# Performance work log

Hardware: AMD Instinct MI355X
Metric: run time of the kernel (lower is better)

The kernel has to match this reference:

```python
import math
import jax, jax.numpy as jnp
import numpy as np

B, DIN, DOUT = 16384, 512, 512
LATERAL_K = 3
K_WTA = max(1, int(DOUT * 0.25))


def _build_L_mask(dout: int, k: int) -> np.ndarray:
    m = np.zeros((dout, dout), dtype=np.float32)
    for j in range(dout):
        nb = []
        for off in range(1, k + 1):
            if j - off >= 0:
                nb.append(j - off)
            if j + off < dout:
                nb.append(j + off)
        for n in nb[:k]:
            m[j, n] = 1.0
    return m


def _kwta_mask(x):
    # top-k winner-take-all mask along last dim (ties resolved like torch.topk)
    _, idx = jax.lax.top_k(x, K_WTA)
    rows = jnp.arange(x.shape[0])[:, None]
    return jnp.zeros_like(x).at[rows, idx].set(1.0)


def _phi(x, mask):
    return jax.nn.gelu(x, approximate=False) * mask


def _phi_deriv(x, mask):
    cdf = 0.5 * (1.0 + jax.lax.erf(x / math.sqrt(2.0)))
    pdf = jnp.exp(-0.5 * x * x) / math.sqrt(2.0 * math.pi)
    return (cdf + x * pdf) * mask


def _clip_update(d, max_norm):
    n = jnp.linalg.norm(d)  # global norm over the whole tensor, as in torch
    return jnp.where(n > max_norm, d * (max_norm / (n + 1e-8)), d)


def setup_inputs() -> dict:
    key = jax.random.key(0)
    ks = jax.random.split(key, 8)
    k_v = math.sqrt(1.0 / DIN)
    k_w = math.sqrt(1.0 / DOUT)
    return {
        "bottom_up": jax.random.normal(ks[0], (B, DIN), jnp.float32),
        "td_target": jax.random.normal(ks[1], (B, DOUT), jnp.float32) * 0.5,
        "x": jax.random.normal(ks[2], (B, DOUT), jnp.float32) * 0.5,
        "V": jax.random.uniform(ks[3], (DIN, DOUT), jnp.float32, -k_v, k_v),
        "b_in": jnp.full((DOUT,), -5.0, jnp.float32),
        "W_snap": jax.random.uniform(ks[4], (DOUT, DIN), jnp.float32, -k_w, k_w),
        "b_out_snap": jnp.zeros((DIN,), jnp.float32),
        "L": jax.random.uniform(ks[5], (DOUT, DOUT), jnp.float32, -0.1, 0.1),
        "L_mask": jnp.asarray(_build_L_mask(DOUT, LATERAL_K)),
        "step_i": 2,
    }


def reference(bottom_up, td_target, x, V, b_in, W_snap, b_out_snap, L, L_mask, step_i):
    tau, eta_x, lambda_act = 0.5, 0.8, 1e-6
    mask = _kwta_mask(x)
    phi_x = _phi(x, mask)                                     # [B, DOUT]
    prediction = phi_x @ W_snap + b_out_snap                  # [B, DIN]
    error = jax.lax.stop_gradient(bottom_up - prediction)     # detached in torch
    feedback_drive = (error @ W_snap.T) * _phi_deriv(x, mask)
    forward_drive = bottom_up @ V + b_in                      # [B, DOUT]
    recognition_drive = forward_drive - x                     # recognition_weight=1.0
    top_down_drive = 3.0 * (td_target - x)
    lateral_drive = phi_x @ (L * L_mask)
    state_grad = (feedback_drive + recognition_drive + top_down_drive
                  + 0.3 * lateral_drive - lambda_act * jnp.sign(x))
    eta = eta_x / (1.0 + 0.1 * step_i)
    dx = _clip_update(tau * eta * state_grad, 1.0)
    return jnp.clip(x + dx, -5.0, 5.0)
```

## Files before the change

### kernel.cpp

```cpp
#include <hip/hip_runtime.h>
#include <hip/hip_bf16.h>
#include <cstdint>


#define DEV static __device__ __forceinline__

typedef __attribute__((ext_vector_type(8))) short short8;
typedef __attribute__((ext_vector_type(4))) float f32x4;

static constexpr int BATCH = 16384;
static constexpr int D = 512;

DEV unsigned short f2bf(float f) {
  unsigned u = __float_as_uint(f);
  return (unsigned short)((u + 0x7FFFu + ((u >> 16) & 1u)) >> 16);
}
DEV float bf2f(unsigned short h) { return __uint_as_float(((unsigned)h) << 16); }

DEV float wsumf(float v) { for (int o = 32; o; o >>= 1) v += __shfl_xor(v, o, 64); return v; }

DEV void gload16(const void* g, void* l) {
  __builtin_amdgcn_global_load_lds((const __attribute__((address_space(1))) void*)g,
                                   (__attribute__((address_space(3))) void*)l, 16, 0, 0);
}

DEV void load8(const float* rowp, int lane, float v[8]) {
  const float4* q = (const float4*)rowp;
  float4 a = q[lane * 2], b = q[lane * 2 + 1];
  v[0] = a.x; v[1] = a.y; v[2] = a.z; v[3] = a.w;
  v[4] = b.x; v[5] = b.y; v[6] = b.z; v[7] = b.w;
}

__global__ __launch_bounds__(256) void prep_k(
    const float* __restrict__ W, const float* __restrict__ V,
    const float* __restrict__ L, const float* __restrict__ Lm,
    unsigned short* __restrict__ Wbt, unsigned short* __restrict__ Wb2,
    unsigned short* __restrict__ Vbt, float* __restrict__ Mc7,
    float* __restrict__ ssq)
{
  int idx = blockIdx.x * 256 + threadIdx.x;
  int n = idx >> 9, k = idx & 511;
  Wbt[idx] = f2bf(W[k * D + n]);
  Wb2[idx] = f2bf(W[idx]);
  Vbt[idx] = f2bf(V[k * D + n]);
  if (idx < 7 * D) {
    int t = idx >> 9, nn = idx & 511;
    int j = nn - 3 + t;
    float v = 0.f;
    if (j >= 0 && j < D && j != nn) v = L[j * D + nn] * Lm[j * D + nn];
    Mc7[idx] = v;
  }
  if (idx == 0) *ssq = 0.f;
}

__global__ __launch_bounds__(256) void kwta_k(
    const float* __restrict__ x, const float* __restrict__ td,
    const float* __restrict__ bu, const float* __restrict__ b_in,
    const float* __restrict__ Mc7,
    unsigned short* __restrict__ phi16, unsigned short* __restrict__ pd16,
    unsigned short* __restrict__ base16, unsigned short* __restrict__ bu16)
{
  __shared__ float pbuf[4][D];
  const int tid = threadIdx.x, lane = tid & 63, wv = tid >> 6;
  const int row = blockIdx.x * 4 + wv;
  const size_t rbase = (size_t)row * D;

  float xv[8];
  load8(x + rbase, lane, xv);
  unsigned key[8];
  #pragma unroll
  for (int s = 0; s < 8; ++s) {
    unsigned u = __float_as_uint(xv[s]);
    key[s] = (u & 0x80000000u) ? ~u : (u | 0x80000000u);
  }
  unsigned T = 0u;
  bool exact = false;
  for (int bit = 31; bit >= 0; --bit) {
    unsigned cand = T | (1u << bit);
    int c = 0;
    #pragma unroll
    for (int s = 0; s < 8; ++s) c += (int)__popcll(__ballot(key[s] >= cand));
    if (c == 128) { T = cand; exact = true; break; }
    if (c > 128) T = cand;
  }

  bool selv[8];
  if (exact) {
    #pragma unroll
    for (int s = 0; s < 8; ++s) selv[s] = (key[s] >= T);
  } else {
    int cg = 0;
    unsigned long long em[8];
    #pragma unroll
    for (int s = 0; s < 8; ++s) {
      cg += (int)__popcll(__ballot(key[s] > T));
      em[s] = __ballot(key[s] == T);
    }
    const int rneed = 128 - cg;
    const unsigned long long lower = (1ull << lane) - 1ull;
    int run = 0;
    #pragma unroll
    for (int s = 0; s < 8; ++s) run += (int)__popcll(em[s] & lower);
    #pragma unroll
    for (int s = 0; s < 8; ++s) {
      bool sel = key[s] > T;
      if (key[s] == T) { sel = (run < rneed); ++run; }
      selv[s] = sel;
    }
  }

  float phiv[8], pdv[8];
  float* pb = pbuf[wv];
  #pragma unroll
  for (int s = 0; s < 8; ++s) {
    float v = xv[s];
    float e  = __expf(-0.5f * v * v);
    float az = fabsf(v) * 0.7071067811865476f;
    float t  = __builtin_amdgcn_rcpf(1.0f + 0.3275911f * az);
    float p  = 0.254829592f + t * (-0.284496736f + t * (1.421413741f +
               t * (-1.453152027f + t * 1.061405429f)));
    float erfa = 1.0f - p * t * e;
    float erfs = (v < 0.f) ? -erfa : erfa;
    float cdf = 0.5f * (1.0f + erfs);
    float ph = selv[s] ? v * cdf : 0.0f;
    float pd = selv[s] ? (cdf + v * 0.3989422804014327f * e) : 0.0f;
    phiv[s] = ph; pdv[s] = pd;
    pb[(s << 6) | lane] = ph;
  }
  __syncthreads();

  float tdv[8], buv[8];
  load8(td + rbase, lane, tdv);
  load8(bu + rbase, lane, buv);

  float lat[8] = {0.f, 0.f, 0.f, 0.f, 0.f, 0.f, 0.f, 0.f};
  #pragma unroll
  for (int t = 0; t < 7; ++t) {
    const float4* mq = (const float4*)(Mc7 + t * D + lane * 8);
    float4 m0 = mq[0], m1 = mq[1];
    float mm[8] = {m0.x, m0.y, m0.z, m0.w, m1.x, m1.y, m1.z, m1.w};
    #pragma unroll
    for (int s = 0; s < 8; ++s) {
      int j = lane * 8 + s - 3 + t;
      int jc = j < 0 ? 0 : (j > D - 1 ? D - 1 : j);
      lat[s] += mm[s] * pb[((jc & 7) << 6) | (jc >> 3)];
    }
  }

  short8 o_phi, o_pd, o_base, o_bu;
  #pragma unroll
  for (int s = 0; s < 8; ++s) {
    int n = lane * 8 + s;
    float v = xv[s];
    float sgn = (v > 0.f) ? 1.f : ((v < 0.f) ? -1.f : 0.f);
    float bs = b_in[n] + 3.f * tdv[s] - 4.f * v + 0.3f * lat[s] - 1e-6f * sgn;
    o_phi[s] = (short)f2bf(phiv[s]);
    o_pd[s]  = (short)f2bf(pdv[s]);
    o_base[s]= (short)f2bf(bs);
    o_bu[s]  = (short)f2bf(buv[s]);
  }
  *(short8*)(phi16 + rbase + lane * 8) = o_phi;
  *(short8*)(pd16  + rbase + lane * 8) = o_pd;
  *(short8*)(base16+ rbase + lane * 8) = o_base;
  *(short8*)(bu16  + rbase + lane * 8) = o_bu;
}

template<int MODE>
__global__ __launch_bounds__(256) void gemm_k(
    const unsigned short* __restrict__ A,
    const unsigned short* __restrict__ Bt,
    const float* __restrict__ f32b,
    const unsigned short* __restrict__ b16a,
    const unsigned short* __restrict__ b16b,
    unsigned short* __restrict__ out16,
    float* __restrict__ ssq,
    const int* __restrict__ stepi)
{
  constexpr int K = 512;
  constexpr int NT = K / 32;
  __shared__ __align__(16) unsigned short As[2][128 * 32];
  __shared__ __align__(16) unsigned short Bs[2][128 * 32];
  const int tid = threadIdx.x;
  const int lane = tid & 63, w = tid >> 6;
  const int lid = (blockIdx.x & 7) * 64 + (blockIdx.x >> 3);
  const int m0 = (lid >> 2) * 128, n0 = (lid & 3) * 128;
  const int qr = (w >> 1) * 64, qc = (w & 1) * 64;
  const int lr = lane & 15, g = lane >> 4;

  f32x4 acc[4][4];
  #pragma unroll
  for (int m = 0; m < 4; ++m)
    #pragma unroll
    for (int n = 0; n < 4; ++n) acc[m][n] = (f32x4){0.f, 0.f, 0.f, 0.f};

  const unsigned short* Abase = A + (size_t)m0 * K;
  const unsigned short* Bbase = Bt + (size_t)n0 * K;

  const int ch0 = tid, ch1 = tid + 256;
  const int r0 = ch0 >> 2, c0 = (ch0 & 3) * 8;
  const int r1 = ch1 >> 2, c1 = (ch1 & 3) * 8;
  auto stage = [&](int buf, int kt) {
    gload16(Abase + r0 * K + kt + c0, As[buf] + (size_t)(w * 64) * 8);
    gload16(Bbase + r0 * K + kt + c0, Bs[buf] + (size_t)(w * 64) * 8);
    gload16(Abase + r1 * K + kt + c1, As[buf] + (size_t)(w * 64 + 256) * 8);
    gload16(Bbase + r1 * K + kt + c1, Bs[buf] + (size_t)(w * 64 + 256) * 8);
  };

  stage(0, 0);
  __syncthreads();
  #pragma unroll
  for (int kt = 0; kt < NT; ++kt) {
    const int cur = kt & 1;
    if (kt + 1 < NT) stage(cur ^ 1, (kt + 1) * 32);
    short8 af[4], bfr[4];
    #pragma unroll
    for (int m = 0; m < 4; ++m) af[m]  = *(const short8*)(As[cur] + (qr + 16 * m + lr) * 32 + 8 * g);
    #pragma unroll
    for (int n = 0; n < 4; ++n) bfr[n] = *(const short8*)(Bs[cur] + (qc + 16 * n + lr) * 32 + 8 * g);
    #pragma unroll
    for (int m = 0; m < 4; ++m)
      #pragma unroll
      for (int n = 0; n < 4; ++n)
        acc[m][n] = __builtin_amdgcn_mfma_f32_16x16x32_bf16(af[m], bfr[n], acc[m][n], 0, 0, 0);
    __syncthreads();
  }

  float tau_eta = 0.f, lssq = 0.f;
  if constexpr (MODE == 3) tau_eta = 0.5f * 0.8f / (1.0f + 0.1f * (float)stepi[0]);
  #pragma unroll
  for (int m = 0; m < 4; ++m) {
    #pragma unroll
    for (int n = 0; n < 4; ++n) {
      #pragma unroll
      for (int r = 0; r < 4; ++r) {
        int row = m0 + qr + 16 * m + 4 * g + r;
        int col = n0 + qc + 16 * n + lr;
        size_t idx = (size_t)row * D + col;
        float v = acc[m][n][r];
        if constexpr (MODE == 1) {
          out16[idx] = f2bf(bf2f(b16a[idx]) - (v + f32b[col]));
        } else if constexpr (MODE == 2) {
          out16[idx] = f2bf(v * bf2f(b16a[idx]));
        } else {
          float dv = tau_eta * (v + bf2f(b16a[idx]) + bf2f(b16b[idx]));
          out16[idx] = f2bf(dv);
          lssq += dv * dv;
        }
      }
    }
  }
  if constexpr (MODE == 3) {
    lssq = wsumf(lssq);
    if (lane == 0) atomicAdd(ssq, lssq);
  }
}

__global__ __launch_bounds__(256) void final_k(const float* __restrict__ x,
                                               const unsigned short* __restrict__ d16,
                                               float* __restrict__ out,
                                               const float* __restrict__ ssq)
{
  float nrm = sqrtf(*ssq);
  float s = nrm > 1.0f ? 1.0f / (nrm + 1e-8f) : 1.0f;
  size_t i = (size_t)blockIdx.x * 256 + threadIdx.x;
  short8 dv = *(const short8*)(d16 + i * 8);
  const float4* xq = (const float4*)(x + i * 8);
  float4 xa = xq[0], xb = xq[1];
  float4 oa, ob;
  oa.x = fminf(fmaxf(xa.x + s * bf2f((unsigned short)dv[0]), -5.f), 5.f);
  oa.y = fminf(fmaxf(xa.y + s * bf2f((unsigned short)dv[1]), -5.f), 5.f);
  oa.z = fminf(fmaxf(xa.z + s * bf2f((unsigned short)dv[2]), -5.f), 5.f);
  oa.w = fminf(fmaxf(xa.w + s * bf2f((unsigned short)dv[3]), -5.f), 5.f);
  ob.x = fminf(fmaxf(xb.x + s * bf2f((unsigned short)dv[4]), -5.f), 5.f);
  ob.y = fminf(fmaxf(xb.y + s * bf2f((unsigned short)dv[5]), -5.f), 5.f);
  ob.z = fminf(fmaxf(xb.z + s * bf2f((unsigned short)dv[6]), -5.f), 5.f);
  ob.w = fminf(fmaxf(xb.w + s * bf2f((unsigned short)dv[7]), -5.f), 5.f);
  float4* oq = (float4*)(out + i * 8);
  oq[0] = oa; oq[1] = ob;
}

extern "C" void kernel_launch(void* const* d_in, const int* in_sizes, int n_in,
                              void* d_out, int out_size, void* d_ws, size_t ws_size,
                              hipStream_t stream) {
  const float* bu    = (const float*)d_in[0];
  const float* td    = (const float*)d_in[1];
  const float* x     = (const float*)d_in[2];
  const float* V     = (const float*)d_in[3];
  const float* b_in  = (const float*)d_in[4];
  const float* W     = (const float*)d_in[5];
  const float* bout  = (const float*)d_in[6];
  const float* L     = (const float*)d_in[7];
  const float* Lm    = (const float*)d_in[8];
  const int*   stepi = (const int*)d_in[9];
  float* dout = (float*)d_out;

  char* p = (char*)d_ws;
  size_t off = 0;
  auto take = [&](size_t bytes) -> void* {
    void* r = (void*)(p + off);
    off += (bytes + 255) & ~(size_t)255;
    return r;
  };
  float* ssq            = (float*)take(4);
  unsigned short* Wbt   = (unsigned short*)take((size_t)D * D * 2);
  unsigned short* Wb2   = (unsigned short*)take((size_t)D * D * 2);
  unsigned short* Vbt   = (unsigned short*)take((size_t)D * D * 2);
  float* Mc7            = (float*)take((size_t)7 * D * 4);
  const size_t bd = (size_t)BATCH * D * 2;
  unsigned short* phi16 = (unsigned short*)take(bd);
  unsigned short* bu16  = (unsigned short*)take(bd);
  unsigned short* pd16  = (unsigned short*)take(bd);
  unsigned short* bse16 = (unsigned short*)take(bd);
  unsigned short* err16 = (unsigned short*)take(bd);
  unsigned short* fb16  = phi16;
  unsigned short* d16   = err16;

  prep_k<<<(D * D) / 256, 256, 0, stream>>>(W, V, L, Lm, Wbt, Wb2, Vbt, Mc7, ssq);
  kwta_k<<<BATCH / 4, 256, 0, stream>>>(x, td, bu, b_in, Mc7, phi16, pd16, bse16, bu16);
  gemm_k<1><<<(BATCH / 128) * (D / 128), 256, 0, stream>>>(
      phi16, Wbt, bout, bu16, nullptr, err16, nullptr, nullptr);
  gemm_k<2><<<(BATCH / 128) * (D / 128), 256, 0, stream>>>(
      err16, Wb2, nullptr, pd16, nullptr, fb16, nullptr, nullptr);
  gemm_k<3><<<(BATCH / 128) * (D / 128), 256, 0, stream>>>(
      bu16, Vbt, nullptr, fb16, bse16, d16, ssq, stepi);
  final_k<<<BATCH * D / 8 / 256, 256, 0, stream>>>(x, d16, dout, ssq);
}
```

Baseline: 278.7 us.

## Deepen GEMM LDS pipeline to four buffers with prefetch distance two

Replaces the double-buffered LDS staging in the GEMM kernel with a four-slot ring that keeps two tiles of loads in flight. Each iteration waits on a partial vmcnt and issues a single barrier instead of a full __syncthreads after compute. The goal is to hide global-to-LDS latency behind the MFMA work. LDS use doubles to 64KB per block, which can lower occupancy, and the hand-written vmcnt counts and the single barrier per step have to line up with the ring reuse pattern for correctness.

```diff
diff --git a/kernel.cpp b/kernel.cpp
--- a/kernel.cpp
+++ b/kernel.cpp
@@ -178,8 +178,8 @@
 {
   constexpr int K = 512;
   constexpr int NT = K / 32;
-  __shared__ __align__(16) unsigned short As[2][128 * 32];
-  __shared__ __align__(16) unsigned short Bs[2][128 * 32];
+  __shared__ __align__(16) unsigned short As[4][128 * 32];
+  __shared__ __align__(16) unsigned short Bs[4][128 * 32];
   const int tid = threadIdx.x;
   const int lane = tid & 63, w = tid >> 6;
   const int lid = (blockIdx.x & 7) * 64 + (blockIdx.x >> 3);
@@ -196,34 +196,44 @@
   const unsigned short* Abase = A + (size_t)m0 * K;
   const unsigned short* Bbase = Bt + (size_t)n0 * K;
 
-  const int ch0 = tid, ch1 = tid + 256;
-  const int r0 = ch0 >> 2, c0 = (ch0 & 3) * 8;
+  const int r0 = tid >> 2, c0 = (tid & 3) * 8;
+  const int ch1 = tid + 256;
   const int r1 = ch1 >> 2, c1 = (ch1 & 3) * 8;
+
   auto stage = [&](int buf, int kt) {
-    gload16(Abase + r0 * K + kt + c0, As[buf] + (size_t)(w * 64) * 8);
-    gload16(Bbase + r0 * K + kt + c0, Bs[buf] + (size_t)(w * 64) * 8);
-    gload16(Abase + r1 * K + kt + c1, As[buf] + (size_t)(w * 64 + 256) * 8);
-    gload16(Bbase + r1 * K + kt + c1, Bs[buf] + (size_t)(w * 64 + 256) * 8);
+    gload16(Abase + (size_t)r0 * K + kt + c0, As[buf] + (w * 64) * 8);
+    gload16(Bbase + (size_t)r0 * K + kt + c0, Bs[buf] + (w * 64) * 8);
+    gload16(Abase + (size_t)r1 * K + kt + c1, As[buf] + (w * 64 + 256) * 8);
+    gload16(Bbase + (size_t)r1 * K + kt + c1, Bs[buf] + (w * 64 + 256) * 8);
   };
-
-  stage(0, 0);
-  __syncthreads();
-  #pragma unroll
-  for (int kt = 0; kt < NT; ++kt) {
-    const int cur = kt & 1;
-    if (kt + 1 < NT) stage(cur ^ 1, (kt + 1) * 32);
+  auto compute = [&](int buf) {
     short8 af[4], bfr[4];
     #pragma unroll
-    for (int m = 0; m < 4; ++m) af[m]  = *(const short8*)(As[cur] + (qr + 16 * m + lr) * 32 + 8 * g);
-    #pragma unroll
-    for (int n = 0; n < 4; ++n) bfr[n] = *(const short8*)(Bs[cur] + (qc + 16 * n + lr) * 32 + 8 * g);
+    for (int m = 0; m < 4; ++m) af[m]  = *(const short8*)(As[buf] + (qr + 16 * m + lr) * 32 + 8 * g);
+    #pragma unroll
+    for (int n = 0; n < 4; ++n) bfr[n] = *(const short8*)(Bs[buf] + (qc + 16 * n + lr) * 32 + 8 * g);
     #pragma unroll
     for (int m = 0; m < 4; ++m)
       #pragma unroll
       for (int n = 0; n < 4; ++n)
         acc[m][n] = __builtin_amdgcn_mfma_f32_16x16x32_bf16(af[m], bfr[n], acc[m][n], 0, 0, 0);
-    __syncthreads();
-  }
+  };
+
+  stage(0, 0);
+  stage(1, 32);
+  #pragma unroll
+  for (int t = 0; t < NT - 2; ++t) {
+    stage((t + 2) & 3, (t + 2) * 32);
+    asm volatile("s_waitcnt vmcnt(8)" ::: "memory");
+    __builtin_amdgcn_s_barrier();
+    compute(t & 3);
+  }
+  asm volatile("s_waitcnt vmcnt(4)" ::: "memory");
+  __builtin_amdgcn_s_barrier();
+  compute((NT - 2) & 3);
+  asm volatile("s_waitcnt vmcnt(0)" ::: "memory");
+  __builtin_amdgcn_s_barrier();
+  compute((NT - 1) & 3);
 
   float tau_eta = 0.f, lssq = 0.f;
   if constexpr (MODE == 3) tau_eta = 0.5f * 0.8f / (1.0f + 0.1f * (float)stepi[0]);
```

Measured after the change: 252.1 us. -9.5%, faster.
